# Kernel tuning notes

Hardware: AMD Instinct MI355X
Metric: run time of the kernel (lower is better)

Reference implementation:

```python
import jax, jax.numpy as jnp
import numpy as np

B, L = 4, 2048
D_Q = D_K = D_V = 512
D_MODEL = 512
H = 8  # heads; head dim = D_MODEL // H = 64


def _conv1x1(x, W, b):
    # Conv1d with kernel_size=1 == pointwise linear over channels.
    # x: (B, C_in, L), W: (C_out, C_in), b: (C_out,) -> (B, C_out, L)
    return jnp.einsum('oc,bcl->bol', W, x) + b[None, :, None]


def setup_inputs() -> dict:
    key = jax.random.key(0)
    ks = jax.random.split(key, 12)
    s = 0.02
    return {
        'q': jax.random.normal(ks[0], (B, D_Q, L), jnp.float32),
        'k': jax.random.normal(ks[1], (B, D_K, L), jnp.float32),
        'v': jax.random.normal(ks[2], (B, D_V, L), jnp.float32),
        'input_mask': jnp.ones((B, 1, L), jnp.float32),
        'Wq': jax.random.normal(ks[3], (D_MODEL, D_Q), jnp.float32) * s,
        'bq': jax.random.normal(ks[4], (D_MODEL,), jnp.float32) * s,
        'Wk': jax.random.normal(ks[5], (D_MODEL, D_K), jnp.float32) * s,
        'bk': jax.random.normal(ks[6], (D_MODEL,), jnp.float32) * s,
        'Wv': jax.random.normal(ks[7], (D_MODEL, D_V), jnp.float32) * s,
        'bv': jax.random.normal(ks[8], (D_MODEL,), jnp.float32) * s,
        'Wout': jax.random.normal(ks[9], (D_V, D_MODEL), jnp.float32) * s,
        'bout': jax.random.normal(ks[10], (D_V,), jnp.float32) * s,
    }


def reference(q, k, v, input_mask, Wq, bq, Wk, bk, Wv, bv, Wout, bout):
    Bq, _, Lq = q.shape
    qh = _conv1x1(q, Wq, bq).reshape(Bq, H, -1, Lq)  # (B,H,D,L)
    kh = _conv1x1(k, Wk, bk).reshape(Bq, H, -1, Lq)
    vh = _conv1x1(v, Wv, bv).reshape(Bq, H, -1, Lq)
    Dh = qh.shape[2]
    scale = 1.0 / jnp.sqrt(jnp.asarray(Dh, qh.dtype))
    scores = jnp.einsum('bhdl,bhdn->bhln', qh, kh) * scale  # (B,H,L,L)
    # total_mask = ~input_mask[:, 0:1, :].bool(); True -> masked keys
    pad = input_mask[:, 0:1, :] <= 0.5  # (B,1,L_k)
    scores = jnp.where(pad[:, None, :, :], jnp.asarray(-1e9, scores.dtype), scores)
    attn = jax.nn.softmax(scores, axis=-1)  # attn_dropout is None in module
    out = jnp.einsum('bhdn,bhln->bhdl', vh, attn).reshape(Bq, -1, Lq)  # (B,d_model,L)
    # self.dropout is identity at inference; final 1x1 conv projection
    return _conv1x1(out, Wout, bout)  # (B, d_v, L)
```

## Files before the change

kernel.cpp:

```cpp
#include <hip/hip_runtime.h>
#include <hip/hip_bf16.h>


#define BB  4
#define LL  2048
#define CC  512
#define HH  8
#define DHH 64

typedef __attribute__((ext_vector_type(8)))  short bf16x8;
typedef __attribute__((ext_vector_type(4)))  short bf16x4;
typedef __attribute__((ext_vector_type(16))) float f32x16;
typedef __attribute__((ext_vector_type(2)))  unsigned uint2v;
typedef __attribute__((ext_vector_type(4)))  unsigned uint4v;

using us = unsigned short;

#if __has_builtin(__builtin_amdgcn_exp2f)
#define EXP2(x) __builtin_amdgcn_exp2f(x)
#else
#define EXP2(x) __expf(0.6931471805599453f * (x))
#endif

__device__ __forceinline__ int swz(int r) { return (r + (r >> 3)) & 7; }

__device__ __forceinline__ us f2bu(float x) {
    unsigned u = __float_as_uint(x);
    return (us)((u + 0x7FFFu + ((u >> 16) & 1u)) >> 16);
}
__device__ __forceinline__ unsigned pk2(float a, float b) {
    unsigned r;
    asm("v_cvt_pk_bf16_f32 %0, %1, %2" : "=v"(r) : "v"(a), "v"(b));
    return r;
}
__device__ __forceinline__ bf16x4 pk4(float a, float b, float c, float d) {
    uint2v u; u[0] = pk2(a, b); u[1] = pk2(c, d);
    return __builtin_bit_cast(bf16x4, u);
}

__device__ __forceinline__ void transpose_body(const float* __restrict__ X,
                                               us* __restrict__ Xt,
                                               int b, int c0, int n0, int t)
{
    __shared__ float T[64][65];

    const float* Xb = X + ((size_t)b * CC + c0) * LL + n0;
    #pragma unroll
    for (int i = 0; i < 4; ++i) {
        const int cl = (t >> 4) + 16 * i, nl = (t & 15) * 4;
        const float4 f = *(const float4*)(Xb + (size_t)cl * LL + nl);
        T[cl][nl + 0] = f.x; T[cl][nl + 1] = f.y;
        T[cl][nl + 2] = f.z; T[cl][nl + 3] = f.w;
    }
    __syncthreads();
    us* Ot = Xt + ((size_t)b * LL + n0) * CC + c0;
    #pragma unroll
    for (int i = 0; i < 2; ++i) {
        const int nl = (t >> 3) + 32 * i, cb = (t & 7) * 8;
        uint4v u;
        #pragma unroll
        for (int j = 0; j < 4; ++j)
            u[j] = pk2(T[cb + 2 * j][nl], T[cb + 2 * j + 1][nl]);
        *(bf16x8*)(Ot + (size_t)nl * CC + cb) = __builtin_bit_cast(bf16x8, u);
    }
}

__global__ __launch_bounds__(256) void transpose_cvt(const float* __restrict__ X,
                                                     us* __restrict__ Xt)
{
    transpose_body(X, Xt, blockIdx.z, blockIdx.y * 64, blockIdx.x * 64, threadIdx.x);
}

__global__ __launch_bounds__(256) void transpose_cvt3(
    const float* __restrict__ Xq, const float* __restrict__ Xk,
    const float* __restrict__ Xv,
    us* __restrict__ X0, us* __restrict__ X1, us* __restrict__ X2)
{
    const int z = blockIdx.z, which = z >> 2, b = z & 3;
    const float* X = which == 0 ? Xq : (which == 1 ? Xk : Xv);
    us* Xt = which == 0 ? X0 : (which == 1 ? X1 : X2);
    transpose_body(X, Xt, b, blockIdx.y * 64, blockIdx.x * 64, threadIdx.x);
}

__global__ __launch_bounds__(256) void cvt_w4(const float* __restrict__ W0,
                                              const float* __restrict__ W1,
                                              const float* __restrict__ W2,
                                              const float* __restrict__ W3,
                                              us* __restrict__ out)
{
    const float* Ws[4] = {W0, W1, W2, W3};
    const float* W = Ws[blockIdx.y];
    us* O = out + (size_t)blockIdx.y * (CC * CC);
    const int i = (blockIdx.x * 256 + threadIdx.x) * 8;
    const float4 f0 = *(const float4*)(W + i);
    const float4 f1 = *(const float4*)(W + i + 4);
    uint4v u;
    u[0] = pk2(f0.x, f0.y); u[1] = pk2(f0.z, f0.w);
    u[2] = pk2(f1.x, f1.y); u[3] = pk2(f1.z, f1.w);
    *(bf16x8*)(O + i) = __builtin_bit_cast(bf16x8, u);
}

__device__ __forceinline__ void proj_body(const us* __restrict__ Xb,
                                          const us* __restrict__ Wm,
                                          const float* __restrict__ bias,
                                          float scale, void* __restrict__ Yv,
                                          int b, int n0, int m0, int t, int mode)
{
    const int lane = t & 63, wave = t >> 6;
    const int quad2 = lane >> 5, l31 = lane & 31;
    const int wm = (wave >> 1) * 32, wn = (wave & 1) * 64;

    __shared__ us As[2][64 * 64];
    __shared__ us Bs[2][128 * 64];
    __shared__ float biasS[64];

    f32x16 acc[2];
    #pragma unroll
    for (int nt = 0; nt < 2; ++nt)
        #pragma unroll
        for (int e = 0; e < 16; ++e) acc[nt][e] = 0.f;

    if (t < 64) biasS[t] = bias[m0 + t];

    #pragma unroll
    for (int i = 0; i < 2; ++i) {
        const int id = i * 256 + t, r = id >> 3, bk = id & 7;
        *(bf16x8*)(As[0] + r * 64 + ((bk ^ swz(r)) * 8)) =
            *(const bf16x8*)(Wm + (size_t)r * CC + bk * 8);
    }
    #pragma unroll
    for (int i = 0; i < 4; ++i) {
        const int id = i * 256 + t, r = id >> 3, bk = id & 7;
        *(bf16x8*)(Bs[0] + r * 64 + ((bk ^ swz(r)) * 8)) =
            *(const bf16x8*)(Xb + (size_t)(n0 + r) * CC + bk * 8);
    }
    __syncthreads();

    for (int it = 0; it < CC / 64; ++it) {
        const int cur = it & 1, k1 = (it + 1) * 64;

        bf16x8 apre[2], bpre[4];
        if (it + 1 < CC / 64) {
            #pragma unroll
            for (int i = 0; i < 2; ++i) {
                const int id = i * 256 + t, r = id >> 3, bk = id & 7;
                apre[i] = *(const bf16x8*)(Wm + (size_t)r * CC + k1 + bk * 8);
            }
            #pragma unroll
            for (int i = 0; i < 4; ++i) {
                const int id = i * 256 + t, r = id >> 3, bk = id & 7;
                bpre[i] = *(const bf16x8*)(Xb + (size_t)(n0 + r) * CC + k1 + bk * 8);
            }
        }

        __builtin_amdgcn_s_setprio(1);
        #pragma unroll
        for (int ks = 0; ks < 4; ++ks) {
            const int bk = quad2 + 2 * ks;
            const int ra = wm + l31;
            const bf16x8 af = *(const bf16x8*)(As[cur] + ra * 64 + ((bk ^ swz(ra)) * 8));
            #pragma unroll
            for (int nt = 0; nt < 2; ++nt) {
                const int rb = wn + nt * 32 + l31;
                const bf16x8 bfr = *(const bf16x8*)(Bs[cur] + rb * 64 + ((bk ^ swz(rb)) * 8));
                acc[nt] = __builtin_amdgcn_mfma_f32_32x32x16_bf16(af, bfr, acc[nt], 0, 0, 0);
            }
        }
        __builtin_amdgcn_s_setprio(0);

        if (it + 1 < CC / 64) {
            #pragma unroll
            for (int i = 0; i < 2; ++i) {
                const int id = i * 256 + t, r = id >> 3, bk = id & 7;
                *(bf16x8*)(As[1 - cur] + r * 64 + ((bk ^ swz(r)) * 8)) = apre[i];
            }
            #pragma unroll
            for (int i = 0; i < 4; ++i) {
                const int id = i * 256 + t, r = id >> 3, bk = id & 7;
                *(bf16x8*)(Bs[1 - cur] + r * 64 + ((bk ^ swz(r)) * 8)) = bpre[i];
            }
        }
        __syncthreads();
    }

    #pragma unroll
    for (int nt = 0; nt < 2; ++nt) {
        const int nloc = wn + nt * 32 + l31;
        if (mode == 0) {
            us* Y = (us*)Yv;
            #pragma unroll
            for (int rg2 = 0; rg2 < 4; ++rg2) {
                const int rbase = wm + 8 * rg2 + 4 * quad2;
                float v0 = (acc[nt][rg2 * 4 + 0] + biasS[rbase + 0]) * scale;
                float v1 = (acc[nt][rg2 * 4 + 1] + biasS[rbase + 1]) * scale;
                float v2 = (acc[nt][rg2 * 4 + 2] + biasS[rbase + 2]) * scale;
                float v3 = (acc[nt][rg2 * 4 + 3] + biasS[rbase + 3]) * scale;
                const int mg = m0 + rbase;
                const int h = mg >> 6, d = mg & 63;
                *(bf16x4*)(Y + (((size_t)(b * HH + h) * LL) + n0 + nloc) * DHH + d) =
                    pk4(v0, v1, v2, v3);
            }
        } else {
            #pragma unroll
            for (int reg = 0; reg < 16; ++reg) {
                const int row = (reg & 3) + 8 * (reg >> 2) + 4 * quad2;
                const int mloc = wm + row;
                const float v = (acc[nt][reg] + biasS[mloc]) * scale;
                const size_t addr = ((size_t)b * CC + m0 + mloc) * LL + n0 + nloc;
                if (mode == 1) ((us*)Yv)[addr] = f2bu(v);
                else           ((float*)Yv)[addr] = v;
            }
        }
    }
}

template <int MODE>
__global__ __launch_bounds__(256, 2) void proj_gemm(const us* __restrict__ Xt,
                                                    const us* __restrict__ Wb,
                                                    const float* __restrict__ bias,
                                                    float scale,
                                                    void* __restrict__ Yv)
{
    const int b = blockIdx.z, n0 = blockIdx.x * 128, m0 = blockIdx.y * 64;
    proj_body(Xt + (size_t)b * LL * CC, Wb + (size_t)m0 * CC, bias, scale, Yv,
              b, n0, m0, threadIdx.x, MODE);
}

__global__ __launch_bounds__(256, 2) void proj_gemm3(
    const us* __restrict__ X0, const us* __restrict__ X1, const us* __restrict__ X2,
    const us* __restrict__ Wb4,
    const float* __restrict__ bq, const float* __restrict__ bk,
    const float* __restrict__ bv, float scale_q,
    us* __restrict__ qh, us* __restrict__ kh, us* __restrict__ vh)
{
    const int z = blockIdx.z, which = z >> 2, b = z & 3;
    const int n0 = blockIdx.x * 128, m0 = blockIdx.y * 64;
    const us* Xt = which == 0 ? X0 : (which == 1 ? X1 : X2);
    const us* Wb = Wb4 + (size_t)which * (CC * CC);
    const float* bias = which == 0 ? bq : (which == 1 ? bk : bv);
    const float scale = which == 0 ? scale_q : 1.0f;
    us* Yv = which == 0 ? qh : (which == 1 ? kh : vh);
    const int mode = (which == 2) ? 1 : 0;
    proj_body(Xt + (size_t)b * LL * CC, Wb + (size_t)m0 * CC, bias, scale,
              (void*)Yv, b, n0, m0, threadIdx.x, mode);
}

__global__ __launch_bounds__(256, 2) void attn_fwd(
    const us* __restrict__ Qh,
    const us* __restrict__ Kh,
    const us* __restrict__ Vh,
    const float* __restrict__ mask,
    us* __restrict__ ctx)
{
    const int bh = blockIdx.x;
    const int b = bh >> 3, h = bh & 7;
    const int qb = blockIdx.y;
    const int t = threadIdx.x, lane = t & 63, wave = t >> 6;
    const int quad2 = lane >> 5, l31 = lane & 31;
    const int qg = qb * 128 + wave * 32;

    __shared__ us Ks[2][64 * 64];
    __shared__ us Vs[2][64 * 64];
    __shared__ unsigned long long mwS[32];

    const float* mb = mask + (size_t)b * LL;
    #pragma unroll
    for (int i = 0; i < 8; ++i) {
        const int tile = wave * 8 + i;
        const unsigned long long bal = __ballot(mb[tile * 64 + lane] > 0.5f);
        if (lane == 0) mwS[tile] = bal;
    }

    const us* Qbase = Qh + (size_t)bh * LL * DHH;
    bf16x8 qf[4];
    #pragma unroll
    for (int ks = 0; ks < 4; ++ks)
        qf[ks] = *(const bf16x8*)(Qbase + (size_t)(qg + l31) * DHH + ks * 16 + quad2 * 8);

    f32x16 of[2];
    #pragma unroll
    for (int mt = 0; mt < 2; ++mt)
        #pragma unroll
        for (int e = 0; e < 16; ++e) of[mt][e] = 0.f;
    float l_run = 0.f;

    const us* Kbase = Kh + (size_t)bh * LL * DHH;
    const us* Vbase = Vh + ((size_t)b * CC + h * DHH) * LL;

    #pragma unroll
    for (int i = 0; i < 2; ++i) {
        const int id = i * 256 + t;
        const int r = id >> 3, bk = id & 7;
        *(bf16x8*)(Ks[0] + r * 64 + ((bk ^ swz(r)) * 8)) =
            *(const bf16x8*)(Kbase + (size_t)r * DHH + bk * 8);
        *(bf16x8*)(Vs[0] + r * 64 + ((bk ^ swz(r)) * 8)) =
            *(const bf16x8*)(Vbase + (size_t)r * LL + bk * 8);
    }
    __syncthreads();

    for (int it = 0; it < LL / 64; ++it) {
        const int cur = it & 1;

        bf16x8 kpre[2], vpre[2];
        if (it + 1 < LL / 64) {
            const int n1 = (it + 1) * 64;
            #pragma unroll
            for (int i = 0; i < 2; ++i) {
                const int id = i * 256 + t;
                const int r = id >> 3, bk = id & 7;
                kpre[i] = *(const bf16x8*)(Kbase + (size_t)(n1 + r) * DHH + bk * 8);
                vpre[i] = *(const bf16x8*)(Vbase + (size_t)r * LL + n1 + bk * 8);
            }
        }

        f32x16 sf[2];
        #pragma unroll
        for (int mt = 0; mt < 2; ++mt)
            #pragma unroll
            for (int e = 0; e < 16; ++e) sf[mt][e] = 0.f;
        __builtin_amdgcn_s_setprio(1);
        #pragma unroll
        for (int ks = 0; ks < 4; ++ks) {
            const int bk = quad2 + 2 * ks;
            #pragma unroll
            for (int mt = 0; mt < 2; ++mt) {
                const int r = mt * 32 + l31;
                const bf16x8 af = *(const bf16x8*)(Ks[cur] + r * 64 + ((bk ^ swz(r)) * 8));
                sf[mt] = __builtin_amdgcn_mfma_f32_32x32x16_bf16(af, qf[ks], sf[mt], 0, 0, 0);
            }
        }
        __builtin_amdgcn_s_setprio(0);

        const unsigned long long mw = mwS[it];
        const bool masked = (mw != 0xFFFFFFFFFFFFFFFFull);
        float ps = 0.f;
        bf16x8 pfrag[4];
        #pragma unroll
        for (int mt = 0; mt < 2; ++mt) {
            float p[16];
            #pragma unroll
            for (int e = 0; e < 16; ++e) p[e] = EXP2(sf[mt][e]);
            if (masked) {
                #pragma unroll
                for (int e = 0; e < 16; ++e) {
                    const int row = 32 * mt + (e & 3) + 8 * (e >> 2) + 4 * quad2;
                    p[e] = ((mw >> row) & 1ull) ? p[e] : 0.f;
                }
            }
            const float s0 = (p[0] + p[1]) + (p[2] + p[3]);
            const float s1 = (p[4] + p[5]) + (p[6] + p[7]);
            const float s2 = (p[8] + p[9]) + (p[10] + p[11]);
            const float s3 = (p[12] + p[13]) + (p[14] + p[15]);
            ps += (s0 + s1) + (s2 + s3);
            #pragma unroll
            for (int g = 0; g < 2; ++g) {
                unsigned w0 = pk2(p[8 * g + 0], p[8 * g + 1]);
                unsigned w1 = pk2(p[8 * g + 2], p[8 * g + 3]);
                unsigned w2 = pk2(p[8 * g + 4], p[8 * g + 5]);
                unsigned w3 = pk2(p[8 * g + 6], p[8 * g + 7]);
                asm("v_permlane32_swap_b32 %0, %1" : "+v"(w0), "+v"(w2));
                asm("v_permlane32_swap_b32 %0, %1" : "+v"(w1), "+v"(w3));
                uint4v u; u[0] = w0; u[1] = w1; u[2] = w2; u[3] = w3;
                pfrag[2 * mt + g] = __builtin_bit_cast(bf16x8, u);
            }
        }
        ps += __shfl_xor(ps, 32, 64);
        l_run += ps;

        __builtin_amdgcn_s_setprio(1);
        #pragma unroll
        for (int ks = 0; ks < 4; ++ks) {
            const int bk = quad2 + 2 * ks;
            #pragma unroll
            for (int mt = 0; mt < 2; ++mt) {
                const int r = mt * 32 + l31;
                const bf16x8 vf = *(const bf16x8*)(Vs[cur] + r * 64 + ((bk ^ swz(r)) * 8));
                of[mt] = __builtin_amdgcn_mfma_f32_32x32x16_bf16(vf, pfrag[ks], of[mt], 0, 0, 0);
            }
        }
        __builtin_amdgcn_s_setprio(0);

        if (it + 1 < LL / 64) {
            #pragma unroll
            for (int i = 0; i < 2; ++i) {
                const int id = i * 256 + t;
                const int r = id >> 3, bk = id & 7;
                *(bf16x8*)(Ks[1 - cur] + r * 64 + ((bk ^ swz(r)) * 8)) = kpre[i];
                *(bf16x8*)(Vs[1 - cur] + r * 64 + ((bk ^ swz(r)) * 8)) = vpre[i];
            }
        }
        __syncthreads();
    }

    us* Cb = ctx + (size_t)b * LL * CC;
    const float inv = 1.0f / l_run;
    const int q = qg + l31;
    #pragma unroll
    for (int mt = 0; mt < 2; ++mt)
        #pragma unroll
        for (int rg2 = 0; rg2 < 4; ++rg2) {
            const int d = 32 * mt + 8 * rg2 + 4 * quad2;
            *(bf16x4*)(Cb + (size_t)q * CC + h * DHH + d) =
                pk4(of[mt][rg2 * 4 + 0] * inv, of[mt][rg2 * 4 + 1] * inv,
                    of[mt][rg2 * 4 + 2] * inv, of[mt][rg2 * 4 + 3] * inv);
        }
}

extern "C" void kernel_launch(void* const* d_in, const int* in_sizes, int n_in,
                              void* d_out, int out_size, void* d_ws, size_t ws_size,
                              hipStream_t stream)
{
    const float* q    = (const float*)d_in[0];
    const float* k    = (const float*)d_in[1];
    const float* v    = (const float*)d_in[2];
    const float* mask = (const float*)d_in[3];
    const float* Wq   = (const float*)d_in[4];
    const float* bq   = (const float*)d_in[5];
    const float* Wk   = (const float*)d_in[6];
    const float* bk   = (const float*)d_in[7];
    const float* Wv   = (const float*)d_in[8];
    const float* bv   = (const float*)d_in[9];
    const float* Wout = (const float*)d_in[10];
    const float* bout = (const float*)d_in[11];

    const size_t TSZ  = (size_t)BB * CC * LL;
    const size_t WSZ  = (size_t)4 * CC * CC;
    const float SCALE_Q = 0.125f * 1.4426950408889634f;

    const dim3 tb(256), gb(256);

    if (ws_size >= (6 * TSZ + WSZ) * sizeof(us)) {
        us* X0  = (us*)d_ws;
        us* X1  = X0 + TSZ;
        us* X2  = X1 + TSZ;
        us* qh  = X2 + TSZ;
        us* kh  = qh + TSZ;
        us* vh  = kh + TSZ;
        us* Wb  = vh + TSZ;
        us* ctx = X0;

        cvt_w4<<<dim3(CC * CC / 2048, 4), tb, 0, stream>>>(Wq, Wk, Wv, Wout, Wb);
        transpose_cvt3<<<dim3(LL / 64, CC / 64, 12), tb, 0, stream>>>(q, k, v, X0, X1, X2);
        proj_gemm3<<<dim3(LL / 128, CC / 64, 12), gb, 0, stream>>>(
            X0, X1, X2, Wb, bq, bk, bv, SCALE_Q, qh, kh, vh);
        attn_fwd<<<dim3(HH * BB, LL / 128), tb, 0, stream>>>(qh, kh, vh, mask, ctx);
        proj_gemm<2><<<dim3(LL / 128, CC / 64, BB), gb, 0, stream>>>(
            ctx, Wb + 3 * (size_t)CC * CC, bout, 1.0f, d_out);
    } else {
        us* Xt  = (us*)d_ws;
        us* qh  = Xt + TSZ;
        us* kh  = qh + TSZ;
        us* vh  = kh + TSZ;
        us* Wb  = vh + TSZ;
        us* ctx = Xt;

        const dim3 tg(LL / 64, CC / 64, BB), gg(LL / 128, CC / 64, BB);

        cvt_w4<<<dim3(CC * CC / 2048, 4), tb, 0, stream>>>(Wq, Wk, Wv, Wout, Wb);
        transpose_cvt<<<tg, tb, 0, stream>>>(q, Xt);
        proj_gemm<0><<<gg, gb, 0, stream>>>(Xt, Wb + 0 * (size_t)CC * CC, bq, SCALE_Q, (void*)qh);
        transpose_cvt<<<tg, tb, 0, stream>>>(k, Xt);
        proj_gemm<0><<<gg, gb, 0, stream>>>(Xt, Wb + 1 * (size_t)CC * CC, bk, 1.0f, (void*)kh);
        transpose_cvt<<<tg, tb, 0, stream>>>(v, Xt);
        proj_gemm<1><<<gg, gb, 0, stream>>>(Xt, Wb + 2 * (size_t)CC * CC, bv, 1.0f, (void*)vh);
        attn_fwd<<<dim3(HH * BB, LL / 128), tb, 0, stream>>>(qh, kh, vh, mask, ctx);
        proj_gemm<2><<<gg, gb, 0, stream>>>(ctx, Wb + 3 * (size_t)CC * CC, bout, 1.0f, d_out);
    }
}
```

Before: 192.5 us.

## Enlarge projection GEMM tiles to 128x128 and prefetch next QK^T in attention

```diff
diff --git a/kernel.cpp b/kernel.cpp
--- a/kernel.cpp
+++ b/kernel.cpp
@@ -108,29 +108,27 @@
 {
     const int lane = t & 63, wave = t >> 6;
     const int quad2 = lane >> 5, l31 = lane & 31;
-    const int wm = (wave >> 1) * 32, wn = (wave & 1) * 64;
-
-    __shared__ us As[2][64 * 64];
+    const int wr = (wave >> 1) * 64, wc = (wave & 1) * 64;
+
+    __shared__ us As[2][128 * 64];
     __shared__ us Bs[2][128 * 64];
-    __shared__ float biasS[64];
-
-    f32x16 acc[2];
-    #pragma unroll
-    for (int nt = 0; nt < 2; ++nt)
-        #pragma unroll
-        for (int e = 0; e < 16; ++e) acc[nt][e] = 0.f;
-
-    if (t < 64) biasS[t] = bias[m0 + t];
-
-    #pragma unroll
-    for (int i = 0; i < 2; ++i) {
+    __shared__ float biasS[128];
+
+    f32x16 acc[2][2];
+    #pragma unroll
+    for (int mi = 0; mi < 2; ++mi)
+        #pragma unroll
+        for (int ni = 0; ni < 2; ++ni)
+            #pragma unroll
+            for (int e = 0; e < 16; ++e) acc[mi][ni][e] = 0.f;
+
+    if (t < 128) biasS[t] = bias[m0 + t];
+
+    #pragma unroll
+    for (int i = 0; i < 4; ++i) {
         const int id = i * 256 + t, r = id >> 3, bk = id & 7;
         *(bf16x8*)(As[0] + r * 64 + ((bk ^ swz(r)) * 8)) =
             *(const bf16x8*)(Wm + (size_t)r * CC + bk * 8);
-    }
-    #pragma unroll
-    for (int i = 0; i < 4; ++i) {
-        const int id = i * 256 + t, r = id >> 3, bk = id & 7;
         *(bf16x8*)(Bs[0] + r * 64 + ((bk ^ swz(r)) * 8)) =
             *(const bf16x8*)(Xb + (size_t)(n0 + r) * CC + bk * 8);
     }
@@ -139,44 +137,38 @@
     for (int it = 0; it < CC / 64; ++it) {
         const int cur = it & 1, k1 = (it + 1) * 64;
 
-        bf16x8 apre[2], bpre[4];
+        bf16x8 apre[4], bpre[4];
         if (it + 1 < CC / 64) {
             #pragma unroll
-            for (int i = 0; i < 2; ++i) {
+            for (int i = 0; i < 4; ++i) {
                 const int id = i * 256 + t, r = id >> 3, bk = id & 7;
                 apre[i] = *(const bf16x8*)(Wm + (size_t)r * CC + k1 + bk * 8);
-            }
+                bpre[i] = *(const bf16x8*)(Xb + (size_t)(n0 + r) * CC + k1 + bk * 8);
+            }
+        }
+
+        __builtin_amdgcn_s_setprio(1);
+        #pragma unroll
+        for (int ks = 0; ks < 4; ++ks) {
+            const int bk = quad2 + 2 * ks;
+            const int ra0 = wr + l31, ra1 = ra0 + 32;
+            const int rb0 = wc + l31, rb1 = rb0 + 32;
+            const bf16x8 af0 = *(const bf16x8*)(As[cur] + ra0 * 64 + ((bk ^ swz(ra0)) * 8));
+            const bf16x8 af1 = *(const bf16x8*)(As[cur] + ra1 * 64 + ((bk ^ swz(ra1)) * 8));
+            const bf16x8 bf0 = *(const bf16x8*)(Bs[cur] + rb0 * 64 + ((bk ^ swz(rb0)) * 8));
+            const bf16x8 bf1 = *(const bf16x8*)(Bs[cur] + rb1 * 64 + ((bk ^ swz(rb1)) * 8));
+            acc[0][0] = __builtin_amdgcn_mfma_f32_32x32x16_bf16(af0, bf0, acc[0][0], 0, 0, 0);
+            acc[0][1] = __builtin_amdgcn_mfma_f32_32x32x16_bf16(af0, bf1, acc[0][1], 0, 0, 0);
+            acc[1][0] = __builtin_amdgcn_mfma_f32_32x32x16_bf16(af1, bf0, acc[1][0], 0, 0, 0);
+            acc[1][1] = __builtin_amdgcn_mfma_f32_32x32x16_bf16(af1, bf1, acc[1][1], 0, 0, 0);
+        }
+        __builtin_amdgcn_s_setprio(0);
+
+        if (it + 1 < CC / 64) {
             #pragma unroll
             for (int i = 0; i < 4; ++i) {
                 const int id = i * 256 + t, r = id >> 3, bk = id & 7;
-                bpre[i] = *(const bf16x8*)(Xb + (size_t)(n0 + r) * CC + k1 + bk * 8);
-            }
-        }
-
-        __builtin_amdgcn_s_setprio(1);
-        #pragma unroll
-        for (int ks = 0; ks < 4; ++ks) {
-            const int bk = quad2 + 2 * ks;
-            const int ra = wm + l31;
-            const bf16x8 af = *(const bf16x8*)(As[cur] + ra * 64 + ((bk ^ swz(ra)) * 8));
-            #pragma unroll
-            for (int nt = 0; nt < 2; ++nt) {
-                const int rb = wn + nt * 32 + l31;
-                const bf16x8 bfr = *(const bf16x8*)(Bs[cur] + rb * 64 + ((bk ^ swz(rb)) * 8));
-                acc[nt] = __builtin_amdgcn_mfma_f32_32x32x16_bf16(af, bfr, acc[nt], 0, 0, 0);
-            }
-        }
-        __builtin_amdgcn_s_setprio(0);
-
-        if (it + 1 < CC / 64) {
-            #pragma unroll
-            for (int i = 0; i < 2; ++i) {
-                const int id = i * 256 + t, r = id >> 3, bk = id & 7;
                 *(bf16x8*)(As[1 - cur] + r * 64 + ((bk ^ swz(r)) * 8)) = apre[i];
-            }
-            #pragma unroll
-            for (int i = 0; i < 4; ++i) {
-                const int id = i * 256 + t, r = id >> 3, bk = id & 7;
                 *(bf16x8*)(Bs[1 - cur] + r * 64 + ((bk ^ swz(r)) * 8)) = bpre[i];
             }
         }
@@ -184,34 +176,36 @@
     }
 
     #pragma unroll
-    for (int nt = 0; nt < 2; ++nt) {
-        const int nloc = wn + nt * 32 + l31;
-        if (mode == 0) {
-            us* Y = (us*)Yv;
-            #pragma unroll
-            for (int rg2 = 0; rg2 < 4; ++rg2) {
-                const int rbase = wm + 8 * rg2 + 4 * quad2;
-                float v0 = (acc[nt][rg2 * 4 + 0] + biasS[rbase + 0]) * scale;
-                float v1 = (acc[nt][rg2 * 4 + 1] + biasS[rbase + 1]) * scale;
-                float v2 = (acc[nt][rg2 * 4 + 2] + biasS[rbase + 2]) * scale;
-                float v3 = (acc[nt][rg2 * 4 + 3] + biasS[rbase + 3]) * scale;
-                const int mg = m0 + rbase;
-                const int h = mg >> 6, d = mg & 63;
-                *(bf16x4*)(Y + (((size_t)(b * HH + h) * LL) + n0 + nloc) * DHH + d) =
-                    pk4(v0, v1, v2, v3);
-            }
-        } else {
-            #pragma unroll
-            for (int reg = 0; reg < 16; ++reg) {
-                const int row = (reg & 3) + 8 * (reg >> 2) + 4 * quad2;
-                const int mloc = wm + row;
-                const float v = (acc[nt][reg] + biasS[mloc]) * scale;
-                const size_t addr = ((size_t)b * CC + m0 + mloc) * LL + n0 + nloc;
-                if (mode == 1) ((us*)Yv)[addr] = f2bu(v);
-                else           ((float*)Yv)[addr] = v;
-            }
-        }
-    }
+    for (int mi = 0; mi < 2; ++mi)
+        #pragma unroll
+        for (int ni = 0; ni < 2; ++ni) {
+            const int nloc = wc + ni * 32 + l31;
+            if (mode == 0) {
+                us* Y = (us*)Yv;
+                #pragma unroll
+                for (int rg2 = 0; rg2 < 4; ++rg2) {
+                    const int rbase = wr + mi * 32 + 8 * rg2 + 4 * quad2;
+                    float v0 = (acc[mi][ni][rg2 * 4 + 0] + biasS[rbase + 0]) * scale;
+                    float v1 = (acc[mi][ni][rg2 * 4 + 1] + biasS[rbase + 1]) * scale;
+                    float v2 = (acc[mi][ni][rg2 * 4 + 2] + biasS[rbase + 2]) * scale;
+                    float v3 = (acc[mi][ni][rg2 * 4 + 3] + biasS[rbase + 3]) * scale;
+                    const int mg = m0 + rbase;
+                    const int h = mg >> 6, d = mg & 63;
+                    *(bf16x4*)(Y + (((size_t)(b * HH + h) * LL) + n0 + nloc) * DHH + d) =
+                        pk4(v0, v1, v2, v3);
+                }
+            } else {
+                #pragma unroll
+                for (int reg = 0; reg < 16; ++reg) {
+                    const int row = (reg & 3) + 8 * (reg >> 2) + 4 * quad2;
+                    const int mloc = wr + mi * 32 + row;
+                    const float v = (acc[mi][ni][reg] + biasS[mloc]) * scale;
+                    const size_t addr = ((size_t)b * CC + m0 + mloc) * LL + n0 + nloc;
+                    if (mode == 1) ((us*)Yv)[addr] = f2bu(v);
+                    else           ((float*)Yv)[addr] = v;
+                }
+            }
+        }
 }
 
 template <int MODE>
@@ -221,7 +215,7 @@
                                                     float scale,
                                                     void* __restrict__ Yv)
 {
-    const int b = blockIdx.z, n0 = blockIdx.x * 128, m0 = blockIdx.y * 64;
+    const int b = blockIdx.z, n0 = blockIdx.x * 128, m0 = blockIdx.y * 128;
     proj_body(Xt + (size_t)b * LL * CC, Wb + (size_t)m0 * CC, bias, scale, Yv,
               b, n0, m0, threadIdx.x, MODE);
 }
@@ -234,7 +228,7 @@
     us* __restrict__ qh, us* __restrict__ kh, us* __restrict__ vh)
 {
     const int z = blockIdx.z, which = z >> 2, b = z & 3;
-    const int n0 = blockIdx.x * 128, m0 = blockIdx.y * 64;
+    const int n0 = blockIdx.x * 128, m0 = blockIdx.y * 128;
     const us* Xt = which == 0 ? X0 : (which == 1 ? X1 : X2);
     const us* Wb = Wb4 + (size_t)which * (CC * CC);
     const float* bias = which == 0 ? bq : (which == 1 ? bk : bv);
@@ -258,6 +252,7 @@
     const int t = threadIdx.x, lane = t & 63, wave = t >> 6;
     const int quad2 = lane >> 5, l31 = lane & 31;
     const int qg = qb * 128 + wave * 32;
+    const int NT = LL / 64;
 
     __shared__ us Ks[2][64 * 64];
     __shared__ us Vs[2][64 * 64];
@@ -298,11 +293,29 @@
     }
     __syncthreads();
 
-    for (int it = 0; it < LL / 64; ++it) {
+    f32x16 sf[2];
+    #pragma unroll
+    for (int mt = 0; mt < 2; ++mt)
+        #pragma unroll
+        for (int e = 0; e < 16; ++e) sf[mt][e] = 0.f;
+    __builtin_amdgcn_s_setprio(1);
+    #pragma unroll
+    for (int ks = 0; ks < 4; ++ks) {
+        const int bk = quad2 + 2 * ks;
+        #pragma unroll
+        for (int mt = 0; mt < 2; ++mt) {
+            const int r = mt * 32 + l31;
+            const bf16x8 af = *(const bf16x8*)(Ks[0] + r * 64 + ((bk ^ swz(r)) * 8));
+            sf[mt] = __builtin_amdgcn_mfma_f32_32x32x16_bf16(af, qf[ks], sf[mt], 0, 0, 0);
+        }
+    }
+    __builtin_amdgcn_s_setprio(0);
+
+    for (int it = 0; it < NT; ++it) {
         const int cur = it & 1;
 
         bf16x8 kpre[2], vpre[2];
-        if (it + 1 < LL / 64) {
+        if (it + 1 < NT) {
             const int n1 = (it + 1) * 64;
             #pragma unroll
             for (int i = 0; i < 2; ++i) {
@@ -312,24 +325,6 @@
                 vpre[i] = *(const bf16x8*)(Vbase + (size_t)r * LL + n1 + bk * 8);
             }
         }
-
-        f32x16 sf[2];
-        #pragma unroll
-        for (int mt = 0; mt < 2; ++mt)
-            #pragma unroll
-            for (int e = 0; e < 16; ++e) sf[mt][e] = 0.f;
-        __builtin_amdgcn_s_setprio(1);
-        #pragma unroll
-        for (int ks = 0; ks < 4; ++ks) {
-            const int bk = quad2 + 2 * ks;
-            #pragma unroll
-            for (int mt = 0; mt < 2; ++mt) {
-                const int r = mt * 32 + l31;
-                const bf16x8 af = *(const bf16x8*)(Ks[cur] + r * 64 + ((bk ^ swz(r)) * 8));
-                sf[mt] = __builtin_amdgcn_mfma_f32_32x32x16_bf16(af, qf[ks], sf[mt], 0, 0, 0);
-            }
-        }
-        __builtin_amdgcn_s_setprio(0);
 
         const unsigned long long mw = mwS[it];
         const bool masked = (mw != 0xFFFFFFFFFFFFFFFFull);
@@ -380,7 +375,7 @@
         }
         __builtin_amdgcn_s_setprio(0);
 
-        if (it + 1 < LL / 64) {
+        if (it + 1 < NT) {
             #pragma unroll
             for (int i = 0; i < 2; ++i) {
                 const int id = i * 256 + t;
@@ -390,6 +385,25 @@
             }
         }
         __syncthreads();
+
+        if (it + 1 < NT) {
+            #pragma unroll
+            for (int mt = 0; mt < 2; ++mt)
+                #pragma unroll
+                for (int e = 0; e < 16; ++e) sf[mt][e] = 0.f;
+            __builtin_amdgcn_s_setprio(1);
+            #pragma unroll
+            for (int ks = 0; ks < 4; ++ks) {
+                const int bk = quad2 + 2 * ks;
+                #pragma unroll
+                for (int mt = 0; mt < 2; ++mt) {
+                    const int r = mt * 32 + l31;
+                    const bf16x8 af = *(const bf16x8*)(Ks[1 - cur] + r * 64 + ((bk ^ swz(r)) * 8));
+                    sf[mt] = __builtin_amdgcn_mfma_f32_32x32x16_bf16(af, qf[ks], sf[mt], 0, 0, 0);
+                }
+            }
+            __builtin_amdgcn_s_setprio(0);
+        }
     }
 
     us* Cb = ctx + (size_t)b * LL * CC;
@@ -441,10 +455,10 @@
 
         cvt_w4<<<dim3(CC * CC / 2048, 4), tb, 0, stream>>>(Wq, Wk, Wv, Wout, Wb);
         transpose_cvt3<<<dim3(LL / 64, CC / 64, 12), tb, 0, stream>>>(q, k, v, X0, X1, X2);
-        proj_gemm3<<<dim3(LL / 128, CC / 64, 12), gb, 0, stream>>>(
+        proj_gemm3<<<dim3(LL / 128, CC / 128, 12), gb, 0, stream>>>(
             X0, X1, X2, Wb, bq, bk, bv, SCALE_Q, qh, kh, vh);
         attn_fwd<<<dim3(HH * BB, LL / 128), tb, 0, stream>>>(qh, kh, vh, mask, ctx);
-        proj_gemm<2><<<dim3(LL / 128, CC / 64, BB), gb, 0, stream>>>(
+        proj_gemm<2><<<dim3(LL / 128, CC / 128, BB), gb, 0, stream>>>(
             ctx, Wb + 3 * (size_t)CC * CC, bout, 1.0f, d_out);
     } else {
         us* Xt  = (us*)d_ws;
@@ -454,7 +468,7 @@
         us* Wb  = vh + TSZ;
         us* ctx = Xt;
 
-        const dim3 tg(LL / 64, CC / 64, BB), gg(LL / 128, CC / 64, BB);
+        const dim3 tg(LL / 64, CC / 64, BB), gg(LL / 128, CC / 128, BB);
 
         cvt_w4<<<dim3(CC * CC / 2048, 4), tb, 0, stream>>>(Wq, Wk, Wv, Wout, Wb);
         transpose_cvt<<<tg, tb, 0, stream>>>(q, Xt);
```

Result: no change. 192.6 us (+0.1%).
